# Optimization experiments

Hardware: AMD Instinct MI355X
Metric: run time of the kernel (lower is better)

Reference implementation:

```python
import jax, jax.numpy as jnp
import numpy as np

B, T, D, H, TE = 8, 1024, 1024, 16, 2048  # batch, seq, latent_dim, heads, time_embed_dim
LN_EPS = 1e-5


def layer_norm(x, w, b):
    m = jnp.mean(x, axis=-1, keepdims=True)
    v = jnp.var(x, axis=-1, keepdims=True)
    return (x - m) / jnp.sqrt(v + LN_EPS) * w + b


def setup_inputs() -> dict:
    key = jax.random.key(0)
    ks = jax.random.split(key, 8)
    s = lambda k, sh: (jax.random.normal(k, sh, jnp.float32) * 0.02)
    return dict(
        x=jax.random.normal(ks[0], (B, T, D), jnp.float32),
        emb=jax.random.normal(ks[1], (B, TE), jnp.float32),
        src_mask=jnp.ones((B, T), jnp.float32),
        norm_w=jnp.ones((D,), jnp.float32), norm_b=jnp.zeros((D,), jnp.float32),
        q_w=s(ks[2], (D, D)), q_b=jnp.zeros((D,), jnp.float32),
        k_w=s(ks[3], (D, D)), k_b=jnp.zeros((D,), jnp.float32),
        v_w=s(ks[4], (D, D)), v_b=jnp.zeros((D,), jnp.float32),
        emb_w=s(ks[5], (TE, 2 * D)), emb_b=jnp.zeros((2 * D,), jnp.float32),
        sb_norm_w=jnp.ones((D,), jnp.float32), sb_norm_b=jnp.zeros((D,), jnp.float32),
        out_w=s(ks[6], (D, D)), out_b=jnp.zeros((D,), jnp.float32),
    )


def reference(x, emb, src_mask, norm_w, norm_b, q_w, q_b, k_w, k_b, v_w, v_b,
              emb_w, emb_b, sb_norm_w, sb_norm_b, out_w, out_b):
    Bx, Tx, Dx = x.shape
    # the torch module applies the SAME LayerNorm to x three times; compute once
    xn = layer_norm(x, norm_w, norm_b)                      # [B,T,D]
    q = (xn @ q_w + q_b).reshape(Bx, Tx, H, -1)             # [B,T,H,l]
    k = (xn @ k_w + k_b).reshape(Bx, Tx, H, -1)
    att = jnp.einsum('bnhl,bmhl->bnmh', q, k)               # [B,T,T,H] (no 1/sqrt(d) scaling, as in source)
    mask = src_mask.reshape(Bx, 1, Tx, 1)
    att = att + (1.0 - mask) * -1000000.0
    att = jax.nn.softmax(att, axis=2)                       # softmax over keys (dim m)
    v = ((xn @ v_w + v_b) * src_mask[:, :, None]).reshape(Bx, Tx, H, -1)
    y = jnp.einsum('bnmh,bmhl->bnhl', att, v).reshape(Bx, Tx, Dx)
    # StylizationBlock (dropout is identity in eval)
    e = jax.nn.silu(emb) @ emb_w + emb_b                    # [B,2D]
    scale, shift = jnp.split(e[:, None, :], 2, axis=2)      # each [B,1,D]
    h = layer_norm(y, sb_norm_w, sb_norm_b) * (1.0 + scale) + shift
    h = jax.nn.silu(h) @ out_w + out_b
    return x + h
```

## Files before the change

### kernel.cpp

```cpp
#include <hip/hip_runtime.h>
#include <cstddef>
#include <cstdint>

#define B_SZ 8
#define T_SEQ 1024
#define D_MODEL 1024
#define NH 16
#define HD 64
#define TE_DIM 2048
#define BT_ROWS 8192

typedef short bf16x8 __attribute__((ext_vector_type(8)));
typedef float f32x4 __attribute__((ext_vector_type(4)));

#define MFMA16(a, b, c) __builtin_amdgcn_mfma_f32_16x16x32_bf16(a, b, c, 0, 0, 0)
#define EXP2(x) __builtin_amdgcn_exp2f(x)

__device__ inline unsigned short f2b(float f) {
  union { float f; unsigned u; } v; v.f = f;
  unsigned r = v.u + 0x7FFF + ((v.u >> 16) & 1);
  return (unsigned short)(r >> 16);
}

__device__ inline float b2f(unsigned short u) {
  union { unsigned u; float f; } v; v.u = ((unsigned)u) << 16; return v.f;
}

__device__ inline unsigned cvtpk(float a, float b) {
  unsigned r;
  asm("v_cvt_pk_bf16_f32 %0, %1, %2" : "=v"(r) : "v"(a), "v"(b));
  return r;
}

__device__ inline float max3f(float a, float b, float c) {
  return fmaxf(fmaxf(a, b), c);
}

__device__ inline void gll16(const void* g, void* l) {
  __builtin_amdgcn_global_load_lds(
      (const __attribute__((address_space(1))) unsigned int*)g,
      (__attribute__((address_space(3))) unsigned int*)l, 16, 0, 0);
}

__global__ __launch_bounds__(256) void ln_kernel(
    const float* __restrict__ x, const float* __restrict__ w,
    const float* __restrict__ b, unsigned short* __restrict__ out)
{
  __shared__ float red[8];
  int row = blockIdx.x;
  int tid = threadIdx.x;
  const float* xr = x + (size_t)row * D_MODEL;
  float4 xv = *(const float4*)&xr[tid * 4];
  float s  = xv.x + xv.y + xv.z + xv.w;
  float ss = xv.x*xv.x + xv.y*xv.y + xv.z*xv.z + xv.w*xv.w;
  #pragma unroll
  for (int off = 32; off; off >>= 1) {
    s  += __shfl_xor(s, off);
    ss += __shfl_xor(ss, off);
  }
  int wv = tid >> 6;
  if ((tid & 63) == 0) { red[wv] = s; red[4 + wv] = ss; }
  __syncthreads();
  s  = red[0] + red[1] + red[2] + red[3];
  ss = red[4] + red[5] + red[6] + red[7];
  float mean = s * (1.f / D_MODEL);
  float var  = ss * (1.f / D_MODEL) - mean * mean;
  float inv  = rsqrtf(var + 1e-5f);
  float4 w4 = *(const float4*)&w[tid * 4];
  float4 b4 = *(const float4*)&b[tid * 4];
  ushort4 o;
  o.x = f2b((xv.x - mean) * inv * w4.x + b4.x);
  o.y = f2b((xv.y - mean) * inv * w4.y + b4.y);
  o.z = f2b((xv.z - mean) * inv * w4.z + b4.z);
  o.w = f2b((xv.w - mean) * inv * w4.w + b4.w);
  int kg = tid >> 4, cb = (tid >> 1) & 7, e = (tid & 1) * 4;
  int col = kg * 64 + ((cb ^ (row & 7)) * 8) + e;
  *(ushort4*)&out[(size_t)row * D_MODEL + col] = o;
}

__global__ __launch_bounds__(256) void transpose_w4(
    const float* __restrict__ s0, const float* __restrict__ s1,
    const float* __restrict__ s2, const float* __restrict__ s3,
    unsigned short* __restrict__ d0, unsigned short* __restrict__ d1,
    unsigned short* __restrict__ d2, unsigned short* __restrict__ d3)
{
  __shared__ float s[32][33];
  int z = blockIdx.z;
  const float* in = z == 0 ? s0 : z == 1 ? s1 : z == 2 ? s2 : s3;
  unsigned short* out = z == 0 ? d0 : z == 1 ? d1 : z == 2 ? d2 : d3;
  int tx = threadIdx.x & 31, ty = threadIdx.x >> 5;
  int r0 = blockIdx.y * 32, c0 = blockIdx.x * 32;
  #pragma unroll
  for (int rr = 0; rr < 4; ++rr)
    s[ty + rr * 8][tx] = in[(size_t)(r0 + ty + rr * 8) * D_MODEL + c0 + tx];
  __syncthreads();
  int k = r0 + tx;
  int kg = k >> 6, cb = (k >> 3) & 7, e = k & 7;
  #pragma unroll
  for (int rr = 0; rr < 4; ++rr) {
    int n = c0 + ty + rr * 8;
    int col = kg * 64 + ((cb ^ (n & 7)) * 8) + e;
    out[(size_t)n * D_MODEL + col] = f2b(s[tx][ty + rr * 8]);
  }
}

__global__ __launch_bounds__(512, 2) void gemm_qkv8(
    const unsigned short* __restrict__ A, const unsigned short* __restrict__ W,
    const float* __restrict__ b0, const float* __restrict__ b1,
    const float* __restrict__ b2, const float* __restrict__ mask,
    unsigned short* __restrict__ O)
{
  const int K = 1024;
  __shared__ __align__(16) unsigned short SA[3][256 * 64];
  __shared__ __align__(16) unsigned short SB[3][128 * 64];
  int tid = threadIdx.x;
  int wid = tid >> 6, lane = tid & 63, g = lane >> 4, lq = lane & 15;
  int wm = wid >> 1, wn = wid & 1;
  int bid = blockIdx.x;
  int xcd = bid & 7, ii = bid >> 3;
  int mt = xcd * 4 + (ii & 3), nt = ii >> 2;
  int m0 = mt * 256;
  int wg = nt >> 3;
  int n0 = (nt & 7) * 128;
  const unsigned short* Bt = W + ((size_t)wg << 20);
  const float* bias = wg == 0 ? b0 : wg == 1 ? b1 : b2;

  f32x4 acc[4][4];
  #pragma unroll
  for (int i = 0; i < 4; ++i)
    #pragma unroll
    for (int j = 0; j < 4; ++j)
      acc[i][j] = (f32x4){0.f, 0.f, 0.f, 0.f};

  const unsigned short* aSrc = A + (size_t)(m0 + (tid >> 3)) * K + (tid & 7) * 8;
  const unsigned short* bSrc = Bt + (size_t)(n0 + (tid >> 3)) * K + (tid & 7) * 8;

  #define STAGE8(slot, t)                                                      \
    {                                                                          \
      size_t ko = (size_t)(t) * 64;                                            \
      _Pragma("unroll")                                                        \
      for (int i2 = 0; i2 < 4; ++i2)                                           \
        gll16(aSrc + ko + (size_t)i2 * 64 * K,                                 \
              (char*)&SA[slot][0] + tid * 16 + i2 * 8192);                     \
      _Pragma("unroll")                                                        \
      for (int i2 = 0; i2 < 2; ++i2)                                           \
        gll16(bSrc + ko + (size_t)i2 * 64 * K,                                 \
              (char*)&SB[slot][0] + tid * 16 + i2 * 8192);                     \
    }

  STAGE8(0, 0)
  STAGE8(1, 1)
  asm volatile("s_waitcnt vmcnt(6)" ::: "memory");
  asm volatile("s_barrier" ::: "memory");

  int cA0 = (g ^ (lq & 7)) * 16;
  int cA1 = ((4 + g) ^ (lq & 7)) * 16;

  #pragma unroll
  for (int t = 0; t < 16; ++t) {
    const char* sa = (const char*)&SA[t % 3][0];
    const char* sb = (const char*)&SB[t % 3][0];
    bf16x8 af[4][2], bf[4][2];
    #pragma unroll
    for (int i = 0; i < 4; ++i) {
      int ra = wm * 64 + i * 16 + lq;
      af[i][0] = *(const bf16x8*)(sa + ra * 128 + cA0);
      af[i][1] = *(const bf16x8*)(sa + ra * 128 + cA1);
      int rb = wn * 64 + i * 16 + lq;
      bf[i][0] = *(const bf16x8*)(sb + rb * 128 + cA0);
      bf[i][1] = *(const bf16x8*)(sb + rb * 128 + cA1);
    }
    if (t < 14) {
      STAGE8((t + 2) % 3, t + 2)
      asm volatile("s_waitcnt vmcnt(6)" ::: "memory");
    } else if (t == 14) {
      asm volatile("s_waitcnt vmcnt(0)" ::: "memory");
    }
    __builtin_amdgcn_s_setprio(1);
    #pragma unroll
    for (int i = 0; i < 4; ++i)
      #pragma unroll
      for (int j = 0; j < 4; ++j) {
        acc[i][j] = MFMA16(af[i][0], bf[j][0], acc[i][j]);
        acc[i][j] = MFMA16(af[i][1], bf[j][1], acc[i][j]);
      }
    __builtin_amdgcn_s_setprio(0);
    if (t < 15) asm volatile("s_barrier" ::: "memory");
  }
  #undef STAGE8

  int colbase = n0 + wn * 64;
  #pragma unroll
  for (int i = 0; i < 4; ++i) {
    int mrow0 = m0 + wm * 64 + i * 16 + g * 4;
    #pragma unroll
    for (int j = 0; j < 4; ++j) {
      int n = colbase + j * 16 + lq;
      float bv = bias[n];
      int h = n >> 6, dd = n & 63;
      if (wg < 2) {
        float scale = wg == 0 ? 1.44269504f : 1.0f;
        unsigned short* Cb = O + ((size_t)wg << 23);
        #pragma unroll
        for (int rr = 0; rr < 4; ++rr) {
          int m = mrow0 + rr;
          int b = m >> 10, tt = m & 1023;
          Cb[((size_t)((b * NH + h) * T_SEQ + tt)) * HD + dd] = f2b((acc[i][j][rr] + bv) * scale);
        }
      } else {
        unsigned short* Cb = O + ((size_t)2 << 23);
        int b = mrow0 >> 10, tt = mrow0 & 1023;
        ushort4 pk;
        unsigned short* pp = (unsigned short*)&pk;
        #pragma unroll
        for (int rr = 0; rr < 4; ++rr)
          pp[rr] = f2b((acc[i][j][rr] + bv) * mask[mrow0 + rr]);
        *(ushort4*)&Cb[((size_t)((b * NH + h) * HD + dd)) * T_SEQ + tt] = pk;
      }
    }
  }
}

__global__ __launch_bounds__(256) void gemm_out(
    const unsigned short* __restrict__ A, const unsigned short* __restrict__ Bt,
    const float* __restrict__ bias, const float* __restrict__ resid,
    float* __restrict__ C)
{
  const int K = 1024;
  __shared__ __align__(16) unsigned short As[128 * 64];
  __shared__ __align__(16) unsigned short Bs[128 * 64];
  int l = blockIdx.x;
  int xcd = l & 7, ii = l >> 3;
  int mt = xcd * 8 + (ii & 7), nt = ii >> 3;
  int m0 = mt * 128, n0 = nt * 128;

  int tid = threadIdx.x;
  int lane = tid & 63, w = tid >> 6;
  int g = lane >> 4, lq = lane & 15;
  int wr = w >> 1, wc = w & 1;
  f32x4 acc[4][4];
  #pragma unroll
  for (int i = 0; i < 4; ++i)
    #pragma unroll
    for (int j = 0; j < 4; ++j)
      acc[i][j] = (f32x4){0.f, 0.f, 0.f, 0.f};

  const unsigned short* aSrc = A + (size_t)(m0 + (tid >> 3)) * K + (tid & 7) * 8;
  const unsigned short* bSrc = Bt + (size_t)(n0 + (tid >> 3)) * K + (tid & 7) * 8;
  char* aDst = (char*)As + tid * 16;
  char* bDst = (char*)Bs + tid * 16;

  for (int k0 = 0; k0 < K; k0 += 64) {
    #pragma unroll
    for (int it = 0; it < 4; ++it) {
      gll16(aSrc + k0 + it * 32 * K, aDst + it * 4096);
      gll16(bSrc + k0 + it * 32 * K, bDst + it * 4096);
    }
    __syncthreads();
    #pragma unroll
    for (int kh = 0; kh < 2; ++kh) {
      bf16x8 af[4], bfr[4];
      #pragma unroll
      for (int i = 0; i < 4; ++i) {
        int ra = wr * 64 + i * 16 + lq;
        af[i] = *(const bf16x8*)((const char*)As + ra * 128 + (((kh * 4 + g) ^ (ra & 7)) * 16));
        int rb = wc * 64 + i * 16 + lq;
        bfr[i] = *(const bf16x8*)((const char*)Bs + rb * 128 + (((kh * 4 + g) ^ (rb & 7)) * 16));
      }
      #pragma unroll
      for (int i = 0; i < 4; ++i)
        #pragma unroll
        for (int j = 0; j < 4; ++j)
          acc[i][j] = MFMA16(af[i], bfr[j], acc[i][j]);
    }
    __syncthreads();
  }

  int colbase = n0 + wc * 64;
  #pragma unroll
  for (int i = 0; i < 4; ++i) {
    int mrow0 = m0 + wr * 64 + i * 16 + g * 4;
    #pragma unroll
    for (int j = 0; j < 4; ++j) {
      int n = colbase + j * 16 + lq;
      float bv = bias[n];
      #pragma unroll
      for (int rr = 0; rr < 4; ++rr) {
        int m = mrow0 + rr;
        C[(size_t)m * D_MODEL + n] = acc[i][j][rr] + bv + resid[(size_t)m * D_MODEL + n];
      }
    }
  }
}

__global__ __launch_bounds__(256) void emb_partial(
    const float* __restrict__ emb, const float* __restrict__ emb_w,
    float* __restrict__ partial)
{
  __shared__ float ses[B_SZ][32];
  int tid = threadIdx.x;
  int t0 = blockIdx.y * 32;
  int n = blockIdx.x * 1024 + tid * 4;
  {
    int b = tid >> 5, t = tid & 31;
    float v = emb[b * TE_DIM + t0 + t];
    ses[b][t] = v / (1.f + __expf(-v));
  }
  __syncthreads();
  f32x4 acc[B_SZ];
  #pragma unroll
  for (int b = 0; b < B_SZ; ++b) acc[b] = (f32x4){0.f, 0.f, 0.f, 0.f};
  #pragma unroll 4
  for (int t = 0; t < 32; ++t) {
    f32x4 wv = *(const f32x4*)&emb_w[(size_t)(t0 + t) * (2 * D_MODEL) + n];
    #pragma unroll
    for (int b = 0; b < B_SZ; ++b) {
      float s = ses[b][t];
      acc[b][0] = fmaf(s, wv[0], acc[b][0]);
      acc[b][1] = fmaf(s, wv[1], acc[b][1]);
      acc[b][2] = fmaf(s, wv[2], acc[b][2]);
      acc[b][3] = fmaf(s, wv[3], acc[b][3]);
    }
  }
  #pragma unroll
  for (int b = 0; b < B_SZ; ++b)
    *(f32x4*)&partial[((size_t)blockIdx.y * B_SZ + b) * (2 * D_MODEL) + n] = acc[b];
}

__global__ __launch_bounds__(256) void emb_reduce(
    const float* __restrict__ partial, const float* __restrict__ emb_b,
    float* __restrict__ e)
{
  int idx = blockIdx.x * 256 + threadIdx.x;
  int b = idx >> 11, n = idx & 2047;
  float acc = emb_b[n];
  #pragma unroll 8
  for (int kb = 0; kb < 64; ++kb)
    acc += partial[((size_t)kb * B_SZ + b) * (2 * D_MODEL) + n];
  e[b * (2 * D_MODEL) + n] = acc;
}

__global__ __launch_bounds__(256, 2) void attn_mfma7(
    const unsigned short* __restrict__ Q, const unsigned short* __restrict__ K,
    const unsigned short* __restrict__ Vt, const float* __restrict__ mask,
    unsigned short* __restrict__ y)
{
  __shared__ __align__(16) unsigned short SM[32768];
  unsigned short* Kb = SM;
  unsigned short* Vb = SM + 8192;
  unsigned short* Pb = SM + 16384;

  int tid = threadIdx.x, w = tid >> 6, lane = tid & 63;
  int g = lane >> 4, lq = lane & 15;
  int bid = blockIdx.x;
  int lid = (bid & 7) * 64 + (bid >> 3);
  int qb = lid & 3, h = (lid >> 2) & 15, b = lid >> 6;
  int q0 = qb * 256 + w * 64;
  size_t hb = ((size_t)(b * NH + h)) * T_SEQ * HD;

  bf16x8 bq[4][2];
  #pragma unroll
  for (int qa = 0; qa < 4; ++qa)
    #pragma unroll
    for (int kh = 0; kh < 2; ++kh)
      bq[qa][kh] = *(const bf16x8*)(Q + hb + (size_t)(q0 + qa * 16 + lq) * HD + kh * 32 + g * 8);

  bf16x8 ones;
  #pragma unroll
  for (int i = 0; i < 8; ++i) ones[i] = (short)16256;

  const char* kBase = (const char*)(K + hb) + lq * 128 + g * 16;
  const char* vBase = (const char*)(Vt + hb) + lq * 2048 + g * 16;
  int c0 = 2 * w, c1 = 2 * w + 1;
  const char* kS0 = kBase + (c0 >> 1) * 2048 + (c0 & 1) * 64;
  const char* kS1 = kBase + (c1 >> 1) * 2048 + (c1 & 1) * 64;
  const char* vS0 = vBase + (c0 >> 1) * 32768 + (c0 & 1) * 64;
  const char* vS1 = vBase + (c1 >> 1) * 32768 + (c1 & 1) * 64;

  f32x4 o[4][4];
  f32x4 osum[4];
  #pragma unroll
  for (int qa = 0; qa < 4; ++qa) {
    osum[qa] = (f32x4){0.f, 0.f, 0.f, 0.f};
    #pragma unroll
    for (int dt = 0; dt < 4; ++dt)
      o[dt][qa] = (f32x4){0.f, 0.f, 0.f, 0.f};
  }
  float mrun[4] = {-3.0e38f, -3.0e38f, -3.0e38f, -3.0e38f};
  const float* maskb = mask + b * T_SEQ;

  gll16(kS0, Kb + c0 * 512);
  gll16(kS1, Kb + c1 * 512);
  gll16(vS0, Vb + c0 * 512);
  gll16(vS1, Vb + c1 * 512);
  __syncthreads();

  for (int t = 0; t < 16; ++t) {
    int cur = t & 1;
    int kv0 = t * 64;
    if (t < 15) {
      int nxt = cur ^ 1;
      size_t ko = (size_t)(kv0 + 64) * 128;
      size_t vo = (size_t)(kv0 + 64) * 2;
      gll16(kS0 + ko, Kb + nxt * 4096 + c0 * 512);
      gll16(kS1 + ko, Kb + nxt * 4096 + c1 * 512);
      gll16(vS0 + vo, Vb + nxt * 4096 + c0 * 512);
      gll16(vS1 + vo, Vb + nxt * 4096 + c1 * 512);
    }
    const unsigned short* Kc = Kb + cur * 4096;
    const unsigned short* Vc = Vb + cur * 4096;

    f32x4 mbv[4];
    #pragma unroll
    for (int kt = 0; kt < 4; ++kt) {
      float4 mk = *(const float4*)&maskb[kv0 + kt * 16 + g * 4];
      mbv[kt][0] = fmaf(mk.x, 1500000.f, -1500000.f);
      mbv[kt][1] = fmaf(mk.y, 1500000.f, -1500000.f);
      mbv[kt][2] = fmaf(mk.z, 1500000.f, -1500000.f);
      mbv[kt][3] = fmaf(mk.w, 1500000.f, -1500000.f);
    }

    bf16x8 kf[4][2];
    #pragma unroll
    for (int kt = 0; kt < 4; ++kt)
      #pragma unroll
      for (int kh = 0; kh < 2; ++kh)
        kf[kt][kh] = *(const bf16x8*)(Kc + (kt * 2 + kh) * 512 + lane * 8);

    f32x4 st[4][4];
    __builtin_amdgcn_s_setprio(1);
    #pragma unroll
    for (int kt = 0; kt < 4; ++kt)
      #pragma unroll
      for (int qa = 0; qa < 4; ++qa) {
        st[kt][qa] = MFMA16(kf[kt][0], bq[qa][0], mbv[kt]);
        st[kt][qa] = MFMA16(kf[kt][1], bq[qa][1], st[kt][qa]);
      }
    __builtin_amdgcn_s_setprio(0);

    bf16x8 vf[4][2];
    #pragma unroll
    for (int dt = 0; dt < 4; ++dt)
      #pragma unroll
      for (int kh = 0; kh < 2; ++kh)
        vf[dt][kh] = *(const bf16x8*)(Vc + (dt * 2 + kh) * 512 + lane * 8);

    float tmax[4];
    #pragma unroll
    for (int qa = 0; qa < 4; ++qa) {
      float m0v = max3f(st[0][qa][0], st[0][qa][1], st[0][qa][2]);
      float m1v = max3f(st[0][qa][3], st[1][qa][0], st[1][qa][1]);
      float m2v = max3f(st[1][qa][2], st[1][qa][3], st[2][qa][0]);
      float m3v = max3f(st[2][qa][1], st[2][qa][2], st[2][qa][3]);
      float m4v = max3f(st[3][qa][0], st[3][qa][1], st[3][qa][2]);
      float t0v = max3f(m0v, m1v, st[3][qa][3]);
      float t1v = max3f(m2v, m3v, m4v);
      float tm = fmaxf(t0v, t1v);
      tm = fmaxf(tm, __shfl_xor(tm, 16));
      tm = fmaxf(tm, __shfl_xor(tm, 32));
      tmax[qa] = tm;
    }
    bool need = false;
    #pragma unroll
    for (int qa = 0; qa < 4; ++qa) need = need || (tmax[qa] > mrun[qa] + 11.5f);
    if (__any((int)need)) {
      #pragma unroll
      for (int qa = 0; qa < 4; ++qa) {
        float mnew = fmaxf(mrun[qa], tmax[qa]);
        float corr = EXP2(mrun[qa] - mnew);
        osum[qa][0] *= corr; osum[qa][1] *= corr;
        osum[qa][2] *= corr; osum[qa][3] *= corr;
        #pragma unroll
        for (int dt = 0; dt < 4; ++dt) {
          o[dt][qa][0] *= corr; o[dt][qa][1] *= corr;
          o[dt][qa][2] *= corr; o[dt][qa][3] *= corr;
        }
        mrun[qa] = mnew;
      }
    }
    #pragma unroll
    for (int qa = 0; qa < 4; ++qa)
      #pragma unroll
      for (int kt = 0; kt < 4; ++kt)
        #pragma unroll
        for (int r = 0; r < 4; ++r)
          st[kt][qa][r] = EXP2(st[kt][qa][r] - mrun[qa]);

    #pragma unroll
    for (int qa = 0; qa < 4; ++qa) {
      unsigned short* Pq = Pb + (w * 4 + qa) * 1024;
      #pragma unroll
      for (int kt = 0; kt < 4; ++kt) {
        uint2 pk2;
        pk2.x = cvtpk(st[kt][qa][0], st[kt][qa][1]);
        pk2.y = cvtpk(st[kt][qa][2], st[kt][qa][3]);
        *(uint2*)((char*)Pq + lq * 128 +
                  (((kt * 2 + (g >> 1)) ^ (lq & 7)) * 16) + (g & 1) * 8) = pk2;
      }
    }

    __builtin_amdgcn_s_setprio(1);
    #pragma unroll
    for (int qa = 0; qa < 4; ++qa) {
      const unsigned short* Pq = Pb + (w * 4 + qa) * 1024;
      #pragma unroll
      for (int kh = 0; kh < 2; ++kh) {
        bf16x8 pa = *(const bf16x8*)((const char*)Pq + lq * 128 +
                                     (((kh * 4 + g) ^ (lq & 7)) * 16));
        osum[qa] = MFMA16(ones, pa, osum[qa]);
        #pragma unroll
        for (int dt = 0; dt < 4; ++dt)
          o[dt][qa] = MFMA16(vf[dt][kh], pa, o[dt][qa]);
      }
    }
    __builtin_amdgcn_s_setprio(0);

    __syncthreads();
  }

  unsigned short* sc = SM + w * 4096;
  #pragma unroll
  for (int qa = 0; qa < 4; ++qa) {
    float inv = 1.f / osum[qa][0];
    #pragma unroll
    for (int dt = 0; dt < 4; ++dt) {
      uint2 pk;
      pk.x = cvtpk(o[dt][qa][0] * inv, o[dt][qa][1] * inv);
      pk.y = cvtpk(o[dt][qa][2] * inv, o[dt][qa][3] * inv);
      *(uint2*)(sc + (qa * 16 + lq) * 64 + dt * 16 + g * 4) = pk;
    }
  }
  #pragma unroll
  for (int it = 0; it < 16; ++it) {
    int row = it * 4 + g;
    ushort4 v = *(const ushort4*)(sc + row * 64 + lq * 4);
    *(ushort4*)&y[(size_t)(b * T_SEQ + q0 + row) * D_MODEL + h * HD + lq * 4] = v;
  }
}

__global__ __launch_bounds__(256) void ln2_kernel(
    const unsigned short* __restrict__ y, const float* __restrict__ w,
    const float* __restrict__ b, const float* __restrict__ e,
    unsigned short* __restrict__ gout)
{
  __shared__ float red[8];
  int row = blockIdx.x;
  int tid = threadIdx.x;
  int bb = row >> 10;
  ushort4 u = *(const ushort4*)&y[(size_t)row * D_MODEL + tid * 4];
  float4 yv = {b2f(u.x), b2f(u.y), b2f(u.z), b2f(u.w)};
  float s  = yv.x + yv.y + yv.z + yv.w;
  float ss = yv.x*yv.x + yv.y*yv.y + yv.z*yv.z + yv.w*yv.w;
  #pragma unroll
  for (int off = 32; off; off >>= 1) {
    s  += __shfl_xor(s, off);
    ss += __shfl_xor(ss, off);
  }
  int wv = tid >> 6;
  if ((tid & 63) == 0) { red[wv] = s; red[4 + wv] = ss; }
  __syncthreads();
  s  = red[0] + red[1] + red[2] + red[3];
  ss = red[4] + red[5] + red[6] + red[7];
  float mean = s * (1.f / D_MODEL);
  float var  = ss * (1.f / D_MODEL) - mean * mean;
  float inv  = rsqrtf(var + 1e-5f);
  float vals[4] = {yv.x, yv.y, yv.z, yv.w};
  ushort4 o;
  unsigned short* op = (unsigned short*)&o;
  #pragma unroll
  for (int j = 0; j < 4; j++) {
    int c = tid * 4 + j;
    float val = (vals[j] - mean) * inv * w[c] + b[c];
    float sc = e[bb * (2 * D_MODEL) + c];
    float sh = e[bb * (2 * D_MODEL) + D_MODEL + c];
    val = val * (1.f + sc) + sh;
    op[j] = f2b(val / (1.f + __expf(-val)));
  }
  int kg = tid >> 4, cb = (tid >> 1) & 7, ee = (tid & 1) * 4;
  int col = kg * 64 + ((cb ^ (row & 7)) * 8) + ee;
  *(ushort4*)&gout[(size_t)row * D_MODEL + col] = o;
}

extern "C" void kernel_launch(void* const* d_in, const int* in_sizes, int n_in,
                              void* d_out, int out_size, void* d_ws, size_t ws_size,
                              hipStream_t stream) {
  const float* x      = (const float*)d_in[0];
  const float* emb    = (const float*)d_in[1];
  const float* mask   = (const float*)d_in[2];
  const float* norm_w = (const float*)d_in[3];
  const float* norm_b = (const float*)d_in[4];
  const float* q_w    = (const float*)d_in[5];
  const float* q_b    = (const float*)d_in[6];
  const float* k_w    = (const float*)d_in[7];
  const float* k_b    = (const float*)d_in[8];
  const float* v_w    = (const float*)d_in[9];
  const float* v_b    = (const float*)d_in[10];
  const float* emb_w  = (const float*)d_in[11];
  const float* emb_b  = (const float*)d_in[12];
  const float* sb_w   = (const float*)d_in[13];
  const float* sb_b   = (const float*)d_in[14];
  const float* out_w  = (const float*)d_in[15];
  const float* out_b  = (const float*)d_in[16];
  float* out = (float*)d_out;

  char* ws = (char*)d_ws;
  const size_t MB = 1u << 20;
  unsigned short* xn   = (unsigned short*)(ws);
  unsigned short* qkv  = (unsigned short*)(ws + 16 * MB);
  unsigned short* qb   = qkv;
  unsigned short* kb   = qkv + (1u << 23);
  unsigned short* vt   = qkv + (2u << 23);
  unsigned short* yb   = (unsigned short*)(ws + 64 * MB);
  unsigned short* gb   = (unsigned short*)(ws + 96 * MB);
  float*          ep   = (float*)(ws + 96 * MB);
  unsigned short* w3t  = (unsigned short*)(ws + 112 * MB);
  unsigned short* owt  = (unsigned short*)(ws + 118 * MB);
  float*          eb   = (float*)(ws + 120 * MB);

  transpose_w4<<<dim3(32, 32, 4), 256, 0, stream>>>(
      q_w, k_w, v_w, out_w,
      w3t, w3t + (1u << 20), w3t + (2u << 20), owt);

  ln_kernel<<<BT_ROWS, 256, 0, stream>>>(x, norm_w, norm_b, xn);

  gemm_qkv8<<<768, 512, 0, stream>>>(xn, w3t, q_b, k_b, v_b, mask, qkv);

  emb_partial<<<dim3(2, 64), 256, 0, stream>>>(emb, emb_w, ep);
  emb_reduce<<<64, 256, 0, stream>>>(ep, emb_b, eb);

  attn_mfma7<<<512, 256, 0, stream>>>(qb, kb, vt, mask, yb);

  ln2_kernel<<<BT_ROWS, 256, 0, stream>>>(yb, sb_w, sb_b, eb, gb);

  gemm_out<<<512, 256, 0, stream>>>(gb, owt, out_b, x, out);
}
```

Baseline: 193.5 us.

## Split QKV GEMM k-step into two half-phases interleaving A/B prefetch with MFMA

Each 64-wide K step of the QKV projection GEMM now runs as two 32-wide halves. Each half loads its own LDS fragments, issues half of the global-to-LDS prefetch for the stage two steps ahead (A tiles in the first half, B tiles in the second), then runs 16 MFMAs. The aim is to lower register pressure for the fragments and spread global loads more evenly across the MFMA work, in a ping-pong style schedule. The cost is extra s_barriers per iteration, which add synchronisation overhead, and the vmcnt wait accounting now depends on the split issue order.

Result: no change. 195.9 us (median of 2 runs) (+1.2%).

```diff
diff --git a/kernel.cpp b/kernel.cpp
--- a/kernel.cpp
+++ b/kernel.cpp
@@ -135,21 +135,25 @@
   const unsigned short* aSrc = A + (size_t)(m0 + (tid >> 3)) * K + (tid & 7) * 8;
   const unsigned short* bSrc = Bt + (size_t)(n0 + (tid >> 3)) * K + (tid & 7) * 8;
 
-  #define STAGE8(slot, t)                                                      \
+  #define STAGE_A(slot, t)                                                     \
     {                                                                          \
       size_t ko = (size_t)(t) * 64;                                            \
       _Pragma("unroll")                                                        \
       for (int i2 = 0; i2 < 4; ++i2)                                           \
         gll16(aSrc + ko + (size_t)i2 * 64 * K,                                 \
               (char*)&SA[slot][0] + tid * 16 + i2 * 8192);                     \
+    }
+  #define STAGE_B(slot, t)                                                     \
+    {                                                                          \
+      size_t ko = (size_t)(t) * 64;                                            \
       _Pragma("unroll")                                                        \
       for (int i2 = 0; i2 < 2; ++i2)                                           \
         gll16(bSrc + ko + (size_t)i2 * 64 * K,                                 \
               (char*)&SB[slot][0] + tid * 16 + i2 * 8192);                     \
     }
 
-  STAGE8(0, 0)
-  STAGE8(1, 1)
+  STAGE_A(0, 0) STAGE_B(0, 0)
+  STAGE_A(1, 1) STAGE_B(1, 1)
   asm volatile("s_waitcnt vmcnt(6)" ::: "memory");
   asm volatile("s_barrier" ::: "memory");
 
@@ -160,34 +164,56 @@
   for (int t = 0; t < 16; ++t) {
     const char* sa = (const char*)&SA[t % 3][0];
     const char* sb = (const char*)&SB[t % 3][0];
-    bf16x8 af[4][2], bf[4][2];
-    #pragma unroll
-    for (int i = 0; i < 4; ++i) {
-      int ra = wm * 64 + i * 16 + lq;
-      af[i][0] = *(const bf16x8*)(sa + ra * 128 + cA0);
-      af[i][1] = *(const bf16x8*)(sa + ra * 128 + cA1);
-      int rb = wn * 64 + i * 16 + lq;
-      bf[i][0] = *(const bf16x8*)(sb + rb * 128 + cA0);
-      bf[i][1] = *(const bf16x8*)(sb + rb * 128 + cA1);
-    }
-    if (t < 14) {
-      STAGE8((t + 2) % 3, t + 2)
-      asm volatile("s_waitcnt vmcnt(6)" ::: "memory");
-    } else if (t == 14) {
-      asm volatile("s_waitcnt vmcnt(0)" ::: "memory");
-    }
-    __builtin_amdgcn_s_setprio(1);
-    #pragma unroll
-    for (int i = 0; i < 4; ++i)
-      #pragma unroll
-      for (int j = 0; j < 4; ++j) {
-        acc[i][j] = MFMA16(af[i][0], bf[j][0], acc[i][j]);
-        acc[i][j] = MFMA16(af[i][1], bf[j][1], acc[i][j]);
-      }
-    __builtin_amdgcn_s_setprio(0);
-    if (t < 15) asm volatile("s_barrier" ::: "memory");
-  }
-  #undef STAGE8
+
+    {
+      bf16x8 af[4], bf[4];
+      #pragma unroll
+      for (int i = 0; i < 4; ++i) {
+        int ra = wm * 64 + i * 16 + lq;
+        af[i] = *(const bf16x8*)(sa + ra * 128 + cA0);
+        int rb = wn * 64 + i * 16 + lq;
+        bf[i] = *(const bf16x8*)(sb + rb * 128 + cA0);
+      }
+      if (t < 14) STAGE_A((t + 2) % 3, t + 2)
+      asm volatile("s_barrier" ::: "memory");
+      __builtin_amdgcn_s_setprio(1);
+      #pragma unroll
+      for (int i = 0; i < 4; ++i)
+        #pragma unroll
+        for (int j = 0; j < 4; ++j)
+          acc[i][j] = MFMA16(af[i], bf[j], acc[i][j]);
+      __builtin_amdgcn_s_setprio(0);
+      asm volatile("s_barrier" ::: "memory");
+    }
+
+    {
+      bf16x8 af[4], bf[4];
+      #pragma unroll
+      for (int i = 0; i < 4; ++i) {
+        int ra = wm * 64 + i * 16 + lq;
+        af[i] = *(const bf16x8*)(sa + ra * 128 + cA1);
+        int rb = wn * 64 + i * 16 + lq;
+        bf[i] = *(const bf16x8*)(sb + rb * 128 + cA1);
+      }
+      if (t < 14) {
+        STAGE_B((t + 2) % 3, t + 2)
+        asm volatile("s_waitcnt vmcnt(6)" ::: "memory");
+      } else if (t == 14) {
+        asm volatile("s_waitcnt vmcnt(0)" ::: "memory");
+      }
+      asm volatile("s_barrier" ::: "memory");
+      __builtin_amdgcn_s_setprio(1);
+      #pragma unroll
+      for (int i = 0; i < 4; ++i)
+        #pragma unroll
+        for (int j = 0; j < 4; ++j)
+          acc[i][j] = MFMA16(af[i], bf[j], acc[i][j]);
+      __builtin_amdgcn_s_setprio(0);
+      if (t < 15) asm volatile("s_barrier" ::: "memory");
+    }
+  }
+  #undef STAGE_A
+  #undef STAGE_B
 
   int colbase = n0 + wn * 64;
   #pragma unroll
```

## Enlarge QKV GEMM tile to 256x256 with ping-pong quadrant schedule

Applied to the files above, without the earlier changes.

The fused QKV projection GEMM moves from a 256x128 tile with triple buffering to a 256x256 tile with double-buffered A/B halves. Each wave now computes a 128x64 sub-tile in four quadrant phases separated by barriers, and global loads for the next K-step are interleaved between phases. Grid size halves to 384 blocks. The goal is higher arithmetic intensity and better overlap of LDS loads with MFMA, at the cost of more accumulator registers, many more barriers, and fewer blocks to spread across CUs.

Result: slower. 197.5 us (+2.1%).

```diff
diff --git a/kernel.cpp b/kernel.cpp
--- a/kernel.cpp
+++ b/kernel.cpp
@@ -104,30 +104,30 @@
   }
 }
 
-__global__ __launch_bounds__(512, 2) void gemm_qkv8(
+__global__ __launch_bounds__(512, 2) void gemm_qkv8p(
     const unsigned short* __restrict__ A, const unsigned short* __restrict__ W,
     const float* __restrict__ b0, const float* __restrict__ b1,
     const float* __restrict__ b2, const float* __restrict__ mask,
     unsigned short* __restrict__ O)
 {
   const int K = 1024;
-  __shared__ __align__(16) unsigned short SA[3][256 * 64];
-  __shared__ __align__(16) unsigned short SB[3][128 * 64];
+  __shared__ __align__(16) unsigned short SA[2][2][128 * 64];
+  __shared__ __align__(16) unsigned short SB[2][2][128 * 64];
   int tid = threadIdx.x;
   int wid = tid >> 6, lane = tid & 63, g = lane >> 4, lq = lane & 15;
-  int wm = wid >> 1, wn = wid & 1;
+  int wm = wid >> 2, wn = wid & 3;
   int bid = blockIdx.x;
   int xcd = bid & 7, ii = bid >> 3;
   int mt = xcd * 4 + (ii & 3), nt = ii >> 2;
   int m0 = mt * 256;
-  int wg = nt >> 3;
-  int n0 = (nt & 7) * 128;
+  int wg = nt >> 2;
+  int n0 = (nt & 3) * 256;
   const unsigned short* Bt = W + ((size_t)wg << 20);
   const float* bias = wg == 0 ? b0 : wg == 1 ? b1 : b2;
 
-  f32x4 acc[4][4];
-  #pragma unroll
-  for (int i = 0; i < 4; ++i)
+  f32x4 acc[8][4];
+  #pragma unroll
+  for (int i = 0; i < 8; ++i)
     #pragma unroll
     for (int j = 0; j < 4; ++j)
       acc[i][j] = (f32x4){0.f, 0.f, 0.f, 0.f};
@@ -135,64 +135,103 @@
   const unsigned short* aSrc = A + (size_t)(m0 + (tid >> 3)) * K + (tid & 7) * 8;
   const unsigned short* bSrc = Bt + (size_t)(n0 + (tid >> 3)) * K + (tid & 7) * 8;
 
-  #define STAGE8(slot, t)                                                      \
-    {                                                                          \
-      size_t ko = (size_t)(t) * 64;                                            \
+  #define STG_A(slot, t)                                                       \
+    { size_t ko = (size_t)(t) * 64;                                            \
       _Pragma("unroll")                                                        \
-      for (int i2 = 0; i2 < 4; ++i2)                                           \
-        gll16(aSrc + ko + (size_t)i2 * 64 * K,                                 \
-              (char*)&SA[slot][0] + tid * 16 + i2 * 8192);                     \
+      for (int hh = 0; hh < 2; ++hh)                                           \
+        _Pragma("unroll")                                                      \
+        for (int i2 = 0; i2 < 2; ++i2)                                         \
+          gll16(aSrc + ko + (size_t)(hh * 128 + i2 * 64) * K,                  \
+                (char*)&SA[slot][hh][0] + tid * 16 + i2 * 8192); }
+  #define STG_B(slot, t)                                                       \
+    { size_t ko = (size_t)(t) * 64;                                            \
       _Pragma("unroll")                                                        \
-      for (int i2 = 0; i2 < 2; ++i2)                                           \
-        gll16(bSrc + ko + (size_t)i2 * 64 * K,                                 \
-              (char*)&SB[slot][0] + tid * 16 + i2 * 8192);                     \
-    }
-
-  STAGE8(0, 0)
-  STAGE8(1, 1)
-  asm volatile("s_waitcnt vmcnt(6)" ::: "memory");
+      for (int hh = 0; hh < 2; ++hh)                                           \
+        _Pragma("unroll")                                                      \
+        for (int i2 = 0; i2 < 2; ++i2)                                         \
+          gll16(bSrc + ko + (size_t)(hh * 128 + i2 * 64) * K,                  \
+                (char*)&SB[slot][hh][0] + tid * 16 + i2 * 8192); }
+
+  STG_A(0, 0) STG_B(0, 0) STG_A(1, 1)
+  asm volatile("s_waitcnt vmcnt(4)" ::: "memory");
   asm volatile("s_barrier" ::: "memory");
 
-  int cA0 = (g ^ (lq & 7)) * 16;
-  int cA1 = ((4 + g) ^ (lq & 7)) * 16;
-
-  #pragma unroll
+  #pragma unroll 2
   for (int t = 0; t < 16; ++t) {
-    const char* sa = (const char*)&SA[t % 3][0];
-    const char* sb = (const char*)&SB[t % 3][0];
-    bf16x8 af[4][2], bf[4][2];
-    #pragma unroll
-    for (int i = 0; i < 4; ++i) {
-      int ra = wm * 64 + i * 16 + lq;
-      af[i][0] = *(const bf16x8*)(sa + ra * 128 + cA0);
-      af[i][1] = *(const bf16x8*)(sa + ra * 128 + cA1);
-      int rb = wn * 64 + i * 16 + lq;
-      bf[i][0] = *(const bf16x8*)(sb + rb * 128 + cA0);
-      bf[i][1] = *(const bf16x8*)(sb + rb * 128 + cA1);
-    }
+    int slot = t & 1;
+    const char* saH = (const char*)&SA[slot][wm][0];
+    const char* sbH = (const char*)&SB[slot][wn >> 1][0];
+    bf16x8 af[4][2], bf[2][2];
+
+    #define LOAD_A(r)                                                          \
+      _Pragma("unroll")                                                        \
+      for (int iif = 0; iif < 4; ++iif) {                                      \
+        int rh = (r) * 64 + iif * 16 + lq;                                     \
+        _Pragma("unroll")                                                      \
+        for (int kh = 0; kh < 2; ++kh)                                         \
+          af[iif][kh] = *(const bf16x8*)(saH + rh * 128 +                      \
+                        (((kh * 4 + g) ^ (rh & 7)) * 16));                     \
+      }
+    #define LOAD_B(c)                                                          \
+      _Pragma("unroll")                                                        \
+      for (int jjf = 0; jjf < 2; ++jjf) {                                      \
+        int ch = (wn & 1) * 64 + (c) * 32 + jjf * 16 + lq;                     \
+        _Pragma("unroll")                                                      \
+        for (int kh = 0; kh < 2; ++kh)                                         \
+          bf[jjf][kh] = *(const bf16x8*)(sbH + ch * 128 +                      \
+                        (((kh * 4 + g) ^ (ch & 7)) * 16));                     \
+      }
+    #define DO_MFMA(r, c)                                                      \
+      __builtin_amdgcn_s_setprio(1);                                           \
+      _Pragma("unroll")                                                        \
+      for (int iif = 0; iif < 4; ++iif)                                        \
+        _Pragma("unroll")                                                      \
+        for (int jjf = 0; jjf < 2; ++jjf) {                                    \
+          acc[(r)*4+iif][(c)*2+jjf] =                                          \
+            MFMA16(af[iif][0], bf[jjf][0], acc[(r)*4+iif][(c)*2+jjf]);         \
+          acc[(r)*4+iif][(c)*2+jjf] =                                          \
+            MFMA16(af[iif][1], bf[jjf][1], acc[(r)*4+iif][(c)*2+jjf]);         \
+        }                                                                      \
+      __builtin_amdgcn_s_setprio(0);
+
+    if (t < 15) STG_B(slot ^ 1, t + 1)
+    LOAD_A(0) LOAD_B(0)
+    asm volatile("s_barrier" ::: "memory");
+    DO_MFMA(0, 0)
+    asm volatile("s_barrier" ::: "memory");
+
+    LOAD_B(1)
+    asm volatile("s_barrier" ::: "memory");
+    DO_MFMA(0, 1)
+    asm volatile("s_barrier" ::: "memory");
+
+    LOAD_A(1)
+    asm volatile("s_barrier" ::: "memory");
+    DO_MFMA(1, 1)
+    asm volatile("s_barrier" ::: "memory");
+
+    if (t < 14) STG_A(slot, t + 2)
+    LOAD_B(0)
+    asm volatile("s_barrier" ::: "memory");
+    DO_MFMA(1, 0)
     if (t < 14) {
-      STAGE8((t + 2) % 3, t + 2)
-      asm volatile("s_waitcnt vmcnt(6)" ::: "memory");
+      asm volatile("s_waitcnt vmcnt(4)" ::: "memory");
     } else if (t == 14) {
       asm volatile("s_waitcnt vmcnt(0)" ::: "memory");
     }
-    __builtin_amdgcn_s_setprio(1);
-    #pragma unroll
-    for (int i = 0; i < 4; ++i)
-      #pragma unroll
-      for (int j = 0; j < 4; ++j) {
-        acc[i][j] = MFMA16(af[i][0], bf[j][0], acc[i][j]);
-        acc[i][j] = MFMA16(af[i][1], bf[j][1], acc[i][j]);
-      }
-    __builtin_amdgcn_s_setprio(0);
     if (t < 15) asm volatile("s_barrier" ::: "memory");
-  }
-  #undef STAGE8
+
+    #undef LOAD_A
+    #undef LOAD_B
+    #undef DO_MFMA
+  }
+  #undef STG_A
+  #undef STG_B
 
   int colbase = n0 + wn * 64;
   #pragma unroll
-  for (int i = 0; i < 4; ++i) {
-    int mrow0 = m0 + wm * 64 + i * 16 + g * 4;
+  for (int i = 0; i < 8; ++i) {
+    int mrow0 = m0 + wm * 128 + i * 16 + g * 4;
     #pragma unroll
     for (int j = 0; j < 4; ++j) {
       int n = colbase + j * 16 + lq;
@@ -623,7 +662,7 @@
 
   ln_kernel<<<BT_ROWS, 256, 0, stream>>>(x, norm_w, norm_b, xn);
 
-  gemm_qkv8<<<768, 512, 0, stream>>>(xn, w3t, q_b, k_b, v_b, mask, qkv);
+  gemm_qkv8p<<<384, 512, 0, stream>>>(xn, w3t, q_b, k_b, v_b, mask, qkv);
 
   emb_partial<<<dim3(2, 64), 256, 0, stream>>>(emb, emb_w, ep);
   emb_reduce<<<64, 256, 0, stream>>>(ep, emb_b, eb);
```

## Merge small kernels into larger launches to cut launch count

Applied to the files above, without the earlier changes.

Folds LayerNorm and the weight transpose into a single prep kernel, runs the embedding partial GEMV as extra blocks appended to the QKV GEMM grid, and runs the embedding reduction as extra blocks appended to the attention grid. This drops the kernel count from eight to five, removing launch gaps and letting the small kernels overlap with the big ones. The cost is divergent block roles within each kernel. The piggybacked emb blocks inherit the large LDS and launch bounds of their hosts, which may affect scheduling.

After: 180.7 us. 6.6% less time.

```diff
diff --git a/kernel.cpp b/kernel.cpp
--- a/kernel.cpp
+++ b/kernel.cpp
@@ -42,65 +42,66 @@
       (__attribute__((address_space(3))) unsigned int*)l, 16, 0, 0);
 }
 
-__global__ __launch_bounds__(256) void ln_kernel(
-    const float* __restrict__ x, const float* __restrict__ w,
-    const float* __restrict__ b, unsigned short* __restrict__ out)
-{
-  __shared__ float red[8];
-  int row = blockIdx.x;
-  int tid = threadIdx.x;
-  const float* xr = x + (size_t)row * D_MODEL;
-  float4 xv = *(const float4*)&xr[tid * 4];
-  float s  = xv.x + xv.y + xv.z + xv.w;
-  float ss = xv.x*xv.x + xv.y*xv.y + xv.z*xv.z + xv.w*xv.w;
-  #pragma unroll
-  for (int off = 32; off; off >>= 1) {
-    s  += __shfl_xor(s, off);
-    ss += __shfl_xor(ss, off);
-  }
-  int wv = tid >> 6;
-  if ((tid & 63) == 0) { red[wv] = s; red[4 + wv] = ss; }
-  __syncthreads();
-  s  = red[0] + red[1] + red[2] + red[3];
-  ss = red[4] + red[5] + red[6] + red[7];
-  float mean = s * (1.f / D_MODEL);
-  float var  = ss * (1.f / D_MODEL) - mean * mean;
-  float inv  = rsqrtf(var + 1e-5f);
-  float4 w4 = *(const float4*)&w[tid * 4];
-  float4 b4 = *(const float4*)&b[tid * 4];
-  ushort4 o;
-  o.x = f2b((xv.x - mean) * inv * w4.x + b4.x);
-  o.y = f2b((xv.y - mean) * inv * w4.y + b4.y);
-  o.z = f2b((xv.z - mean) * inv * w4.z + b4.z);
-  o.w = f2b((xv.w - mean) * inv * w4.w + b4.w);
-  int kg = tid >> 4, cb = (tid >> 1) & 7, e = (tid & 1) * 4;
-  int col = kg * 64 + ((cb ^ (row & 7)) * 8) + e;
-  *(ushort4*)&out[(size_t)row * D_MODEL + col] = o;
-}
-
-__global__ __launch_bounds__(256) void transpose_w4(
+__global__ __launch_bounds__(256) void prep_kernel(
+    const float* __restrict__ x, const float* __restrict__ norm_w,
+    const float* __restrict__ norm_b, unsigned short* __restrict__ xn,
     const float* __restrict__ s0, const float* __restrict__ s1,
     const float* __restrict__ s2, const float* __restrict__ s3,
     unsigned short* __restrict__ d0, unsigned short* __restrict__ d1,
     unsigned short* __restrict__ d2, unsigned short* __restrict__ d3)
 {
-  __shared__ float s[32][33];
-  int z = blockIdx.z;
-  const float* in = z == 0 ? s0 : z == 1 ? s1 : z == 2 ? s2 : s3;
-  unsigned short* out = z == 0 ? d0 : z == 1 ? d1 : z == 2 ? d2 : d3;
-  int tx = threadIdx.x & 31, ty = threadIdx.x >> 5;
-  int r0 = blockIdx.y * 32, c0 = blockIdx.x * 32;
-  #pragma unroll
-  for (int rr = 0; rr < 4; ++rr)
-    s[ty + rr * 8][tx] = in[(size_t)(r0 + ty + rr * 8) * D_MODEL + c0 + tx];
-  __syncthreads();
-  int k = r0 + tx;
-  int kg = k >> 6, cb = (k >> 3) & 7, e = k & 7;
-  #pragma unroll
-  for (int rr = 0; rr < 4; ++rr) {
-    int n = c0 + ty + rr * 8;
-    int col = kg * 64 + ((cb ^ (n & 7)) * 8) + e;
-    out[(size_t)n * D_MODEL + col] = f2b(s[tx][ty + rr * 8]);
+  __shared__ float red[8];
+  __shared__ float sT[32][33];
+  int bid = blockIdx.x;
+  int tid = threadIdx.x;
+  if (bid < BT_ROWS) {
+    int row = bid;
+    const float* xr = x + (size_t)row * D_MODEL;
+    float4 xv = *(const float4*)&xr[tid * 4];
+    float s  = xv.x + xv.y + xv.z + xv.w;
+    float ss = xv.x*xv.x + xv.y*xv.y + xv.z*xv.z + xv.w*xv.w;
+    #pragma unroll
+    for (int off = 32; off; off >>= 1) {
+      s  += __shfl_xor(s, off);
+      ss += __shfl_xor(ss, off);
+    }
+    int wv = tid >> 6;
+    if ((tid & 63) == 0) { red[wv] = s; red[4 + wv] = ss; }
+    __syncthreads();
+    s  = red[0] + red[1] + red[2] + red[3];
+    ss = red[4] + red[5] + red[6] + red[7];
+    float mean = s * (1.f / D_MODEL);
+    float var  = ss * (1.f / D_MODEL) - mean * mean;
+    float inv  = rsqrtf(var + 1e-5f);
+    float4 w4 = *(const float4*)&norm_w[tid * 4];
+    float4 b4 = *(const float4*)&norm_b[tid * 4];
+    ushort4 o;
+    o.x = f2b((xv.x - mean) * inv * w4.x + b4.x);
+    o.y = f2b((xv.y - mean) * inv * w4.y + b4.y);
+    o.z = f2b((xv.z - mean) * inv * w4.z + b4.z);
+    o.w = f2b((xv.w - mean) * inv * w4.w + b4.w);
+    int kg = tid >> 4, cb = (tid >> 1) & 7, e = (tid & 1) * 4;
+    int col = kg * 64 + ((cb ^ (row & 7)) * 8) + e;
+    *(ushort4*)&xn[(size_t)row * D_MODEL + col] = o;
+  } else {
+    int tb = bid - BT_ROWS;
+    int z = tb >> 10, yy = (tb >> 5) & 31, xx = tb & 31;
+    const float* in = z == 0 ? s0 : z == 1 ? s1 : z == 2 ? s2 : s3;
+    unsigned short* out = z == 0 ? d0 : z == 1 ? d1 : z == 2 ? d2 : d3;
+    int tx = tid & 31, ty = tid >> 5;
+    int r0 = yy * 32, c0 = xx * 32;
+    #pragma unroll
+    for (int rr = 0; rr < 4; ++rr)
+      sT[ty + rr * 8][tx] = in[(size_t)(r0 + ty + rr * 8) * D_MODEL + c0 + tx];
+    __syncthreads();
+    int k = r0 + tx;
+    int kg = k >> 6, cb = (k >> 3) & 7, e = k & 7;
+    #pragma unroll
+    for (int rr = 0; rr < 4; ++rr) {
+      int n = c0 + ty + rr * 8;
+      int col = kg * 64 + ((cb ^ (n & 7)) * 8) + e;
+      out[(size_t)n * D_MODEL + col] = f2b(sT[tx][ty + rr * 8]);
+    }
   }
 }
 
@@ -108,15 +109,50 @@
     const unsigned short* __restrict__ A, const unsigned short* __restrict__ W,
     const float* __restrict__ b0, const float* __restrict__ b1,
     const float* __restrict__ b2, const float* __restrict__ mask,
-    unsigned short* __restrict__ O)
+    unsigned short* __restrict__ O,
+    const float* __restrict__ emb, const float* __restrict__ emb_w,
+    float* __restrict__ partial)
 {
   const int K = 1024;
   __shared__ __align__(16) unsigned short SA[3][256 * 64];
   __shared__ __align__(16) unsigned short SB[3][128 * 64];
   int tid = threadIdx.x;
+  int bid = blockIdx.x;
+
+  if (bid >= 768) {
+    int kb = bid - 768;
+    float* ses = (float*)&SA[0][0];
+    int t0 = kb * 32;
+    if (tid < 256) {
+      int b = tid >> 5, t = tid & 31;
+      float v = emb[b * TE_DIM + t0 + t];
+      ses[b * 32 + t] = v / (1.f + __expf(-v));
+    }
+    __syncthreads();
+    int n = tid * 4;
+    f32x4 acc[B_SZ];
+    #pragma unroll
+    for (int b = 0; b < B_SZ; ++b) acc[b] = (f32x4){0.f, 0.f, 0.f, 0.f};
+    #pragma unroll 4
+    for (int t = 0; t < 32; ++t) {
+      f32x4 wv = *(const f32x4*)&emb_w[(size_t)(t0 + t) * (2 * D_MODEL) + n];
+      #pragma unroll
+      for (int b = 0; b < B_SZ; ++b) {
+        float s = ses[b * 32 + t];
+        acc[b][0] = fmaf(s, wv[0], acc[b][0]);
+        acc[b][1] = fmaf(s, wv[1], acc[b][1]);
+        acc[b][2] = fmaf(s, wv[2], acc[b][2]);
+        acc[b][3] = fmaf(s, wv[3], acc[b][3]);
+      }
+    }
+    #pragma unroll
+    for (int b = 0; b < B_SZ; ++b)
+      *(f32x4*)&partial[((size_t)kb * B_SZ + b) * (2 * D_MODEL) + n] = acc[b];
+    return;
+  }
+
   int wid = tid >> 6, lane = tid & 63, g = lane >> 4, lq = lane & 15;
   int wm = wid >> 1, wn = wid & 1;
-  int bid = blockIdx.x;
   int xcd = bid & 7, ii = bid >> 3;
   int mt = xcd * 4 + (ii & 3), nt = ii >> 2;
   int m0 = mt * 256;
@@ -293,66 +329,34 @@
   }
 }
 
-__global__ __launch_bounds__(256) void emb_partial(
-    const float* __restrict__ emb, const float* __restrict__ emb_w,
-    float* __restrict__ partial)
-{
-  __shared__ float ses[B_SZ][32];
-  int tid = threadIdx.x;
-  int t0 = blockIdx.y * 32;
-  int n = blockIdx.x * 1024 + tid * 4;
-  {
-    int b = tid >> 5, t = tid & 31;
-    float v = emb[b * TE_DIM + t0 + t];
-    ses[b][t] = v / (1.f + __expf(-v));
-  }
-  __syncthreads();
-  f32x4 acc[B_SZ];
-  #pragma unroll
-  for (int b = 0; b < B_SZ; ++b) acc[b] = (f32x4){0.f, 0.f, 0.f, 0.f};
-  #pragma unroll 4
-  for (int t = 0; t < 32; ++t) {
-    f32x4 wv = *(const f32x4*)&emb_w[(size_t)(t0 + t) * (2 * D_MODEL) + n];
-    #pragma unroll
-    for (int b = 0; b < B_SZ; ++b) {
-      float s = ses[b][t];
-      acc[b][0] = fmaf(s, wv[0], acc[b][0]);
-      acc[b][1] = fmaf(s, wv[1], acc[b][1]);
-      acc[b][2] = fmaf(s, wv[2], acc[b][2]);
-      acc[b][3] = fmaf(s, wv[3], acc[b][3]);
-    }
-  }
-  #pragma unroll
-  for (int b = 0; b < B_SZ; ++b)
-    *(f32x4*)&partial[((size_t)blockIdx.y * B_SZ + b) * (2 * D_MODEL) + n] = acc[b];
-}
-
-__global__ __launch_bounds__(256) void emb_reduce(
+__global__ __launch_bounds__(256, 2) void attn_mfma7(
+    const unsigned short* __restrict__ Q, const unsigned short* __restrict__ K,
+    const unsigned short* __restrict__ Vt, const float* __restrict__ mask,
+    unsigned short* __restrict__ y,
     const float* __restrict__ partial, const float* __restrict__ emb_b,
     float* __restrict__ e)
 {
-  int idx = blockIdx.x * 256 + threadIdx.x;
-  int b = idx >> 11, n = idx & 2047;
-  float acc = emb_b[n];
-  #pragma unroll 8
-  for (int kb = 0; kb < 64; ++kb)
-    acc += partial[((size_t)kb * B_SZ + b) * (2 * D_MODEL) + n];
-  e[b * (2 * D_MODEL) + n] = acc;
-}
-
-__global__ __launch_bounds__(256, 2) void attn_mfma7(
-    const unsigned short* __restrict__ Q, const unsigned short* __restrict__ K,
-    const unsigned short* __restrict__ Vt, const float* __restrict__ mask,
-    unsigned short* __restrict__ y)
-{
   __shared__ __align__(16) unsigned short SM[32768];
+  int tid = threadIdx.x;
+  int bid = blockIdx.x;
+
+  if (bid >= 512) {
+    int idx = (bid - 512) * 256 + tid;
+    int b = idx >> 11, n = idx & 2047;
+    float acc = emb_b[n];
+    #pragma unroll 8
+    for (int kb = 0; kb < 64; ++kb)
+      acc += partial[((size_t)kb * B_SZ + b) * (2 * D_MODEL) + n];
+    e[b * (2 * D_MODEL) + n] = acc;
+    return;
+  }
+
   unsigned short* Kb = SM;
   unsigned short* Vb = SM + 8192;
   unsigned short* Pb = SM + 16384;
 
-  int tid = threadIdx.x, w = tid >> 6, lane = tid & 63;
+  int w = tid >> 6, lane = tid & 63;
   int g = lane >> 4, lq = lane & 15;
-  int bid = blockIdx.x;
   int lid = (bid & 7) * 64 + (bid >> 3);
   int qb = lid & 3, h = (lid >> 2) & 15, b = lid >> 6;
   int q0 = qb * 256 + w * 64;
@@ -617,18 +621,15 @@
   unsigned short* owt  = (unsigned short*)(ws + 118 * MB);
   float*          eb   = (float*)(ws + 120 * MB);
 
-  transpose_w4<<<dim3(32, 32, 4), 256, 0, stream>>>(
+  prep_kernel<<<BT_ROWS + 4096, 256, 0, stream>>>(
+      x, norm_w, norm_b, xn,
       q_w, k_w, v_w, out_w,
       w3t, w3t + (1u << 20), w3t + (2u << 20), owt);
 
-  ln_kernel<<<BT_ROWS, 256, 0, stream>>>(x, norm_w, norm_b, xn);
-
-  gemm_qkv8<<<768, 512, 0, stream>>>(xn, w3t, q_b, k_b, v_b, mask, qkv);
-
-  emb_partial<<<dim3(2, 64), 256, 0, stream>>>(emb, emb_w, ep);
-  emb_reduce<<<64, 256, 0, stream>>>(ep, emb_b, eb);
-
-  attn_mfma7<<<512, 256, 0, stream>>>(qb, kb, vt, mask, yb);
+  gemm_qkv8<<<832, 512, 0, stream>>>(xn, w3t, q_b, k_b, v_b, mask, qkv,
+                                     emb, emb_w, ep);
+
+  attn_mfma7<<<576, 256, 0, stream>>>(qb, kb, vt, mask, yb, ep, emb_b, eb);
 
   ln2_kernel<<<BT_ROWS, 256, 0, stream>>>(yb, sb_w, sb_b, eb, gb);
 
```
